# Performance work log

Hardware: AMD Instinct MI355X
Metric: run time of the kernel (lower is better)

## Reference

```python
import jax, jax.numpy as jnp
import numpy as np

N, E, NG = 50000, 800000, 500          # nodes, edges, graphs
HID, HEADS, DH, AIN = 128, 4, 32, 200  # hidden, heads, head dim, atom feat dim
L, NBASE = 5, 1                        # total Roost layers; base layers = roost_layers-3 = 1


def _bn(x, g, b):
    # BatchNorm1d in training mode: batch stats over axis 0 (biased var), affine
    m = x.mean(axis=0)
    v = x.var(axis=0)
    return g * (x - m) * jax.lax.rsqrt(v + 1e-5) + b


def _mlp(x, W, b, g, be):
    # MLPLayer = Linear -> BatchNorm1d -> SiLU
    return jax.nn.silu(_bn(x @ W + b, g, be))


def _roost(x, w, src, dst, Wf, bf, gf, bef, Wg, bg, gg, beg, gn, ben):
    n = x.shape[0]
    hihj = jnp.concatenate([x[src], x[dst]], axis=-1)            # [E, 2h]
    e = jnp.exp(_mlp(hihj, Wf, bf, gf, bef))                     # [E, 1]
    wexp = w[src] * e                                            # [E, 1] src weight * exp(e_ij)
    sum_w = jax.ops.segment_sum(wexp, dst, num_segments=n)       # [N, 1] dst-normalizer
    a = wexp / sum_w[dst]                                        # [E, 1] attention coeff
    z = jnp.einsum('ef,hfd->ehd', hihj, Wg) + bg                 # [E, H, dh] per-head linear
    z = jax.nn.silu(gg * (z - z.mean(axis=0)) * jax.lax.rsqrt(z.var(axis=0) + 1e-5) + beg)
    m = (a[:, :, None] * z).reshape(hihj.shape[0], HID)          # concat heads -> [E, h]
    h = jax.ops.segment_sum(m, dst, num_segments=n)              # scatter-sum to dst nodes
    return _bn(h, gn, ben) + x                                   # bn_nodes + residual


def setup_inputs() -> dict:
    ks = list(jax.random.split(jax.random.key(0), 16))
    f32 = jnp.float32
    return {
        "atom_features": jax.random.normal(ks[0], (N, AIN), f32),
        "node_weight": jax.random.uniform(ks[1], (N, 1), f32, minval=0.05, maxval=1.0),
        "eps": jax.random.normal(ks[2], (N, HID), f32),
        "src": jax.random.randint(ks[3], (E,), 0, N),
        "dst": jax.random.randint(ks[4], (E,), 0, N),
        "graph_ids": jnp.sort(jax.random.randint(ks[5], (N,), 0, NG)),
        "W_embed": jax.random.normal(ks[6], (AIN, HID), f32) / np.sqrt(AIN).astype(np.float32),
        "b_embed": jnp.zeros((HID,), f32),
        "g_embed": jnp.ones((HID,), f32),
        "be_embed": jnp.zeros((HID,), f32),
        "Wf": jax.random.normal(ks[7], (L, 2 * HID, 1), f32) / np.sqrt(2 * HID).astype(np.float32),
        "bf": jnp.zeros((L, 1), f32),
        "gf": jnp.ones((L, 1), f32),
        "bef": jnp.zeros((L, 1), f32),
        "Wg": jax.random.normal(ks[8], (L, HEADS, 2 * HID, DH), f32) / np.sqrt(2 * HID).astype(np.float32),
        "bg": jnp.zeros((L, HEADS, DH), f32),
        "gg": jnp.ones((L, HEADS, DH), f32),
        "beg": jnp.zeros((L, HEADS, DH), f32),
        "gn": jnp.ones((L, HID), f32),
        "ben": jnp.zeros((L, HID), f32),
        "W_mu": jax.random.normal(ks[9], (HID, HID), f32) / np.sqrt(HID).astype(np.float32),
        "b_mu": jnp.zeros((HID,), f32),
        "W_var": jax.random.normal(ks[10], (HID, HID), f32) * 0.01,
        "b_var": jnp.zeros((HID,), f32),
    }


def reference(atom_features, node_weight, eps, W_embed, b_embed, g_embed, be_embed,
              Wf, bf, gf, bef, Wg, bg, gg, beg, gn, ben,
              W_mu, b_mu, W_var, b_var, src, dst, graph_ids):
    x = _mlp(atom_features, W_embed, b_embed, g_embed, be_embed)  # atom_embedding
    for i in range(NBASE):                                        # base_modules
        x = _roost(x, node_weight, src, dst, Wf[i], bf[i], gf[i], bef[i],
                   Wg[i], bg[i], gg[i], beg[i], gn[i], ben[i])
    mu = x @ W_mu + b_mu
    logvar = x @ W_var + b_var
    x = eps * jnp.exp(0.5 * logvar) + mu                          # reparameterize
    for i in range(NBASE, L):                                     # module_layers
        x = _roost(x, node_weight, src, dst, Wf[i], bf[i], gf[i], bef[i],
                   Wg[i], bg[i], gg[i], beg[i], gn[i], ben[i])
    sums = jax.ops.segment_sum(x, graph_ids, num_segments=NG)     # AvgPooling
    cnt = jax.ops.segment_sum(jnp.ones((N,), x.dtype), graph_ids, num_segments=NG)
    xr = sums / jnp.maximum(cnt, 1.0)[:, None]
    kld = jnp.mean(-0.5 * jnp.sum(1.0 + logvar - mu * mu - jnp.exp(logvar), axis=1))
    return xr, kld
```

## Files before the change

kernel.cpp:

```cpp
#include <hip/hip_runtime.h>
#include <hip/hip_bf16.h>
#include <stdint.h>

#define HID 128
#define LAYERS 5

typedef __attribute__((ext_vector_type(8))) short short8;
typedef __attribute__((ext_vector_type(4))) float f32x4;

__device__ __forceinline__ float bf2f(unsigned int u16) {
  union { unsigned int i; float f; } c; c.i = u16 << 16; return c.f;
}
__device__ __forceinline__ unsigned short f2bf(float f) {
  union { float f; unsigned int i; } c; c.f = f;
  unsigned int r = c.i + 0x7fffu + ((c.i >> 16) & 1u);
  return (unsigned short)(r >> 16);
}
__device__ __forceinline__ float fexp(float x) {
  float r; asm("v_exp_f32 %0, %1" : "=v"(r) : "v"(x * 1.44269504f)); return r;
}
__device__ __forceinline__ float frcp(float x) {
  float r; asm("v_rcp_f32 %0, %1" : "=v"(r) : "v"(x)); return r;
}
__device__ __forceinline__ float siluf(float v) { return v * frcp(1.f + fexp(-v)); }

template<int KS, int NCT, bool BF16OUT>
__launch_bounds__(256)
__global__ void gemm_bf16_kernel(const unsigned short* __restrict__ A,
                                 const unsigned short* __restrict__ Bt,
                                 const float* __restrict__ bias,
                                 void* __restrict__ Cv, int M) {
  constexpr int K = KS * 32;
  constexpr int SLOTS = KS * 4;
  constexpr int SSTR = (SLOTS + 7) & ~7;
  __shared__ unsigned short wlds[NCT * 16 * SSTR * 8];
  for (int i = threadIdx.x; i < NCT * 16 * SLOTS; i += 256) {
    int col = i / SLOTS, slot = i % SLOTS;
    int phys = slot ^ (col & 7);
    *(uint4*)&wlds[(col * SSTR + phys) * 8] = *(const uint4*)(Bt + (size_t)col * K + slot * 8);
  }
  __syncthreads();
  int lane = threadIdx.x & 63, wid = threadIdx.x >> 6;
  int l15 = lane & 15, l4 = lane >> 4;
  int n0 = blockIdx.x * 64 + wid * 16;
  f32x4 acc[NCT];
  #pragma unroll
  for (int ct = 0; ct < NCT; ++ct) { f32x4 z = {0.f, 0.f, 0.f, 0.f}; acc[ct] = z; }
  int ar = n0 + l15; if (ar >= M) ar = M - 1;
  #pragma unroll
  for (int kk = 0; kk < KS; ++kk) {
    short8 af = *(const short8*)(A + (size_t)ar * K + kk * 32 + l4 * 8);
    #pragma unroll
    for (int ct = 0; ct < NCT; ++ct) {
      int col = ct * 16 + l15;
      int phys = (kk * 4 + l4) ^ (col & 7);
      short8 bfr = *(const short8*)&wlds[(col * SSTR + phys) * 8];
      acc[ct] = __builtin_amdgcn_mfma_f32_16x16x32_bf16(af, bfr, acc[ct], 0, 0, 0);
    }
  }
  #pragma unroll
  for (int ct = 0; ct < NCT; ++ct) {
    int col = ct * 16 + l15;
    #pragma unroll
    for (int j = 0; j < 4; ++j) {
      int n = n0 + l4 * 4 + j;
      if (n < M) {
        float v = acc[ct][j] + bias[col];
        if (BF16OUT) ((unsigned short*)Cv)[(size_t)n * (NCT * 16) + col] = f2bf(v);
        else         ((float*)Cv)[(size_t)n * (NCT * 16) + col] = v;
      }
    }
  }
}

__global__ void cast_atom_kernel(const float* __restrict__ atom, unsigned short* __restrict__ ab,
                                 int N, int AIN) {
  int n = blockIdx.x, k = threadIdx.x;
  if (n < N && k < 224)
    ab[(size_t)n * 224 + k] = f2bf(k < AIN ? atom[(size_t)n * AIN + k] : 0.f);
}
__global__ void prep_we_kernel(const float* __restrict__ W, unsigned short* __restrict__ Bt,
                               int AIN) {
  int i = blockIdx.x * 256 + threadIdx.x;
  if (i >= 128 * 224) return;
  int col = i / 224, k = i % 224;
  Bt[i] = f2bf(k < AIN ? W[(size_t)k * 128 + col] : 0.f);
}

__global__ void colstats_kernel(const float* __restrict__ in, int M, float* __restrict__ stats) {
  int f = threadIdx.x & 127;
  int rl = threadIdx.x >> 7;
  float s = 0, s2 = 0;
  for (int r = blockIdx.x * 2 + rl; r < M; r += gridDim.x * 2) {
    float v = in[(size_t)r * 128 + f];
    s += v; s2 += v * v;
  }
  __shared__ float l1[256], l2[256];
  l1[threadIdx.x] = s; l2[threadIdx.x] = s2;
  __syncthreads();
  if (rl == 0) {
    atomicAdd(&stats[f],       s  + l1[128 + f]);
    atomicAdd(&stats[128 + f], s2 + l2[128 + f]);
  }
}

template<bool SILU, bool RES>
__global__ void bn_act_kernel(const float* __restrict__ in, const float* __restrict__ stats,
                              const float* __restrict__ g, const float* __restrict__ be,
                              const float* __restrict__ resid, float invM,
                              float* __restrict__ xout, unsigned short* __restrict__ xbout,
                              size_t total) {
  int f = threadIdx.x & 127;
  float mean = stats[f] * invM;
  float var  = stats[128 + f] * invM - mean * mean;
  float sc = g[f] * rsqrtf(var + 1e-5f);
  float sh = be[f] - mean * sc;
  for (size_t i = (size_t)blockIdx.x * blockDim.x + threadIdx.x; i < total;
       i += (size_t)gridDim.x * blockDim.x) {
    float v = in[i] * sc + sh;
    if (SILU) v = siluf(v);
    if (RES)  v += resid[i];
    xout[i] = v;
    xbout[i] = f2bf(v);
  }
}

__global__ void hist_kernel(const int* __restrict__ ids, int* __restrict__ deg, int E) {
  for (int e = blockIdx.x * blockDim.x + threadIdx.x; e < E; e += gridDim.x * blockDim.x)
    atomicAdd(&deg[ids[e]], 1);
}

__global__ void scan_block_kernel(const int* __restrict__ in, int n,
                                  int* __restrict__ excl, int* __restrict__ totals) {
  __shared__ int tmp[256];
  int idx = blockIdx.x * 256 + threadIdx.x;
  int v = (idx < n) ? in[idx] : 0;
  tmp[threadIdx.x] = v;
  __syncthreads();
  for (int o = 1; o < 256; o <<= 1) {
    int t = (threadIdx.x >= o) ? tmp[threadIdx.x - o] : 0;
    __syncthreads();
    tmp[threadIdx.x] += t;
    __syncthreads();
  }
  if (idx < n) excl[idx] = tmp[threadIdx.x] - v;
  if (threadIdx.x == 255 && totals) totals[blockIdx.x] = tmp[255];
}

__global__ void scan_add_kernel(const int* __restrict__ excl, const int* __restrict__ tot_excl,
                                const int* __restrict__ indeg, int* __restrict__ cstart, int n) {
  int idx = blockIdx.x * 256 + threadIdx.x;
  if (idx < n) {
    int v = excl[idx] + tot_excl[blockIdx.x];
    cstart[idx] = v;
    if (idx == n - 1) cstart[n] = v + indeg[idx];
  }
}

__global__ void scatter_kernel(const int* __restrict__ src, const int* __restrict__ dst,
                               const int* __restrict__ cstart, int* __restrict__ fill,
                               int* __restrict__ csrc, int* __restrict__ cdst, int E) {
  for (int e = blockIdx.x * blockDim.x + threadIdx.x; e < E; e += gridDim.x * blockDim.x) {
    int d = dst[e];
    int pos = cstart[d] + atomicAdd(&fill[d], 1);
    csrc[pos] = src[e];
    cdst[pos] = d;
  }
}

__global__ void prep_wg_kernel(const float* __restrict__ WgL, const float* __restrict__ bgL,
                               unsigned short* __restrict__ Bt, float* __restrict__ bias) {
  int i = blockIdx.x * 256 + threadIdx.x;
  if (i < 256 * 128) {
    int col = i >> 7, k = i & 127;
    int c = col & 127, h = c >> 5, d = c & 31;
    int krow = (col < 128) ? k : 128 + k;
    Bt[i] = f2bf(WgL[((size_t)h * 256 + krow) * 32 + d]);
  }
  if (i < 256) bias[i] = (i < 128) ? 0.f : bgL[i - 128];
}

__global__ void prep_mv_kernel(const float* __restrict__ Wm, const float* __restrict__ Wv,
                               const float* __restrict__ bm, const float* __restrict__ bv,
                               unsigned short* __restrict__ Bt, float* __restrict__ bias) {
  int i = blockIdx.x * 256 + threadIdx.x;
  if (i < 256 * 128) {
    int col = i >> 7, k = i & 127;
    Bt[i] = f2bf(col < 128 ? Wm[(size_t)k * 128 + col] : Wv[(size_t)k * 128 + col - 128]);
  }
  if (i < 256) bias[i] = (i < 128) ? bm[i] : bv[i - 128];
}

__global__ void pq_kernel(const float* __restrict__ x, const float* __restrict__ WfL,
                          const float* __restrict__ bfL, float* __restrict__ p,
                          float* __restrict__ q, int N) {
  __shared__ float wf[256];
  wf[threadIdx.x] = WfL[threadIdx.x];
  __syncthreads();
  int wid = threadIdx.x >> 6, lane = threadIdx.x & 63;
  float bf0 = bfL[0];
  for (int n = blockIdx.x * 4 + wid; n < N; n += gridDim.x * 4) {
    float2 xv = *(const float2*)(x + (size_t)n * 128 + lane * 2);
    float pp = xv.x * wf[lane * 2]       + xv.y * wf[lane * 2 + 1];
    float qq = xv.x * wf[128 + lane * 2] + xv.y * wf[129 + lane * 2];
    #pragma unroll
    for (int o = 32; o; o >>= 1) { pp += __shfl_down(pp, o); qq += __shfl_down(qq, o); }
    if (lane == 0) { p[n] = pp; q[n] = qq + bf0; }
  }
}

__global__ void gstat_kernel(const float* __restrict__ p, const float* __restrict__ q,
                             const int* __restrict__ src, const int* __restrict__ dst,
                             float* __restrict__ gstats, int E) {
  float s = 0, s2 = 0;
  for (int e = blockIdx.x * blockDim.x + threadIdx.x; e < E; e += gridDim.x * blockDim.x) {
    float t = p[src[e]] + q[dst[e]];
    s += t; s2 += t * t;
  }
  #pragma unroll
  for (int o = 32; o; o >>= 1) { s += __shfl_down(s, o); s2 += __shfl_down(s2, o); }
  __shared__ float la[4], lb[4];
  int lane = threadIdx.x & 63, wid = threadIdx.x >> 6;
  if (lane == 0) { la[wid] = s; lb[wid] = s2; }
  __syncthreads();
  if (threadIdx.x == 0) {
    atomicAdd(&gstats[0], la[0] + la[1] + la[2] + la[3]);
    atomicAdd(&gstats[1], lb[0] + lb[1] + lb[2] + lb[3]);
  }
}

__global__ void gate_wexp_kernel(const int* __restrict__ cs, const int* __restrict__ csrc,
                                 const float* __restrict__ p, const float* __restrict__ q,
                                 const float* __restrict__ nodew, const float* __restrict__ gstats,
                                 const float* __restrict__ gfL, const float* __restrict__ befL,
                                 float* __restrict__ wexp, float* __restrict__ sum_w,
                                 int N, float invE) {
  float gm  = gstats[0] * invE;
  float gv  = gstats[1] * invE - gm * gm;
  float gsc = gfL[0] * rsqrtf(gv + 1e-5f);
  float gsh = befL[0] - gm * gsc;
  for (int n = blockIdx.x * blockDim.x + threadIdx.x; n < N; n += gridDim.x * blockDim.x) {
    float qn = q[n] * gsc + gsh;
    int s0 = cs[n], s1 = cs[n + 1];
    float sw = 0;
    for (int j = s0; j < s1; ++j) {
      int sn = csrc[j];
      float v = p[sn] * gsc + qn;
      v = v * frcp(1.f + fexp(-v));
      float we = nodew[sn] * fexp(v);
      wexp[j] = we;
      sw += we;
    }
    sum_w[n] = sw;
  }
}

__global__ void zstat_node_kernel(const unsigned short* __restrict__ UVb,
                                  const int* __restrict__ indeg, const int* __restrict__ outdeg,
                                  float* __restrict__ zstats, int N) {
  int lane = threadIdx.x & 63, g = threadIdx.x >> 6;
  int f0 = lane * 2, f1 = f0 + 1;
  float zs0 = 0, zq0 = 0, zs1 = 0, zq1 = 0;
  for (int n = blockIdx.x * 4 + g; n < N; n += gridDim.x * 4) {
    float od = (float)outdeg[n], id = (float)indeg[n];
    unsigned up = *(const unsigned*)(UVb + ((size_t)n << 8) + f0);
    unsigned vp = *(const unsigned*)(UVb + ((size_t)n << 8) + 128 + f0);
    float u0 = bf2f(up & 0xffffu), u1 = bf2f(up >> 16);
    float v0 = bf2f(vp & 0xffffu), v1 = bf2f(vp >> 16);
    zs0 += od * u0 + id * v0;  zq0 += od * u0 * u0 + id * v0 * v0;
    zs1 += od * u1 + id * v1;  zq1 += od * u1 * u1 + id * v1 * v1;
  }
  __shared__ float r1[4][128], r2[4][128];
  r1[g][f0] = zs0; r1[g][f1] = zs1;
  r2[g][f0] = zq0; r2[g][f1] = zq1;
  __syncthreads();
  if (threadIdx.x < 128) {
    int f = threadIdx.x;
    atomicAdd(&zstats[f],       r1[0][f] + r1[1][f] + r1[2][f] + r1[3][f]);
    atomicAdd(&zstats[128 + f], r2[0][f] + r2[1][f] + r2[2][f] + r2[3][f]);
  }
}

__global__ void zcross_kernel(const unsigned short* __restrict__ UVb,
                              const int* __restrict__ csrc, const int* __restrict__ cdst,
                              float* __restrict__ zc_parts, int E) {
  int lane = threadIdx.x & 63;
  int gw = (blockIdx.x * 256 + threadIdx.x) >> 6;
  int nw = (gridDim.x * 256) >> 6;
  int f0 = lane * 2;
  float cr0 = 0, cr1 = 0;
  int nch = (E + 63) >> 6;
  for (int c = gw; c < nch; c += nw) {
    int e0 = c << 6, len = min(64, E - e0);
    int ee = e0 + (lane < len ? lane : len - 1);
    int idxs = csrc[ee], idxd = cdst[ee];
    int dcur = __shfl(idxd, 0);
    float su0 = 0, su1 = 0;
    unsigned up_next = *(const unsigned*)(UVb + ((size_t)__shfl(idxs, 0) << 8) + f0);
    for (int i = 0; i < len; ++i) {
      unsigned up = up_next;
      if (i + 1 < len)
        up_next = *(const unsigned*)(UVb + ((size_t)__shfl(idxs, i + 1) << 8) + f0);
      int d = __shfl(idxd, i);
      if (d != dcur) {
        unsigned vp = *(const unsigned*)(UVb + ((size_t)dcur << 8) + 128 + f0);
        cr0 += bf2f(vp & 0xffffu) * su0; cr1 += bf2f(vp >> 16) * su1;
        su0 = su1 = 0; dcur = d;
      }
      su0 += bf2f(up & 0xffffu); su1 += bf2f(up >> 16);
    }
    unsigned vp = *(const unsigned*)(UVb + ((size_t)dcur << 8) + 128 + f0);
    cr0 += bf2f(vp & 0xffffu) * su0; cr1 += bf2f(vp >> 16) * su1;
  }
  atomicAdd(&zc_parts[(blockIdx.x & 31) * 128 + f0],     cr0);
  atomicAdd(&zc_parts[(blockIdx.x & 31) * 128 + f0 + 1], cr1);
}

__global__ void walk2_kernel(const unsigned short* __restrict__ UVb,
                             const int* __restrict__ csrc, const int* __restrict__ cdst,
                             const float* __restrict__ wexp, const float* __restrict__ sum_w,
                             const float* __restrict__ zstats, const float* __restrict__ zc_parts,
                             const float* __restrict__ gg, const float* __restrict__ beg,
                             float* __restrict__ h, int E, float invE) {
  int lane = threadIdx.x & 63;
  int gw = (blockIdx.x * 256 + threadIdx.x) >> 6;
  int nw = (gridDim.x * 256) >> 6;
  int f0 = lane * 2, f1 = f0 + 1;
  float cr0 = 0, cr1 = 0;
  #pragma unroll
  for (int i2 = 0; i2 < 32; ++i2) { cr0 += zc_parts[i2 * 128 + f0]; cr1 += zc_parts[i2 * 128 + f1]; }
  float zm0 = zstats[f0] * invE;
  float zv0 = (zstats[128 + f0] + 2.f * cr0) * invE - zm0 * zm0;
  float sc0 = gg[f0] * rsqrtf(zv0 + 1e-5f), sh0 = beg[f0] - zm0 * sc0;
  float zm1 = zstats[f1] * invE;
  float zv1 = (zstats[128 + f1] + 2.f * cr1) * invE - zm1 * zm1;
  float sc1 = gg[f1] * rsqrtf(zv1 + 1e-5f), sh1 = beg[f1] - zm1 * sc1;

  int nch = (E + 63) >> 6;
  for (int c = gw; c < nch; c += nw) {
    int e0 = c << 6, len = min(64, E - e0);
    int ee = e0 + (lane < len ? lane : len - 1);
    int idxs = csrc[ee], idxd = cdst[ee];
    float wv = wexp[ee];
    int dcur = __shfl(idxd, 0);
    float inv = frcp(sum_w[dcur]);
    float c0, c1;
    { unsigned vp = *(const unsigned*)(UVb + ((size_t)dcur << 8) + 128 + f0);
      c0 = bf2f(vp & 0xffffu) * sc0 + sh0; c1 = bf2f(vp >> 16) * sc1 + sh1; }
    float h0 = 0, h1 = 0;
    unsigned up_next = *(const unsigned*)(UVb + ((size_t)__shfl(idxs, 0) << 8) + f0);
    for (int i = 0; i < len; ++i) {
      unsigned up = up_next;
      if (i + 1 < len)
        up_next = *(const unsigned*)(UVb + ((size_t)__shfl(idxs, i + 1) << 8) + f0);
      int d = __shfl(idxd, i);
      float a = __shfl(wv, i);
      if (d != dcur) {
        atomicAdd(&h[((size_t)dcur << 7) + f0], h0 * inv);
        atomicAdd(&h[((size_t)dcur << 7) + f1], h1 * inv);
        h0 = h1 = 0; dcur = d; inv = frcp(sum_w[d]);
        unsigned vp = *(const unsigned*)(UVb + ((size_t)d << 8) + 128 + f0);
        c0 = bf2f(vp & 0xffffu) * sc0 + sh0; c1 = bf2f(vp >> 16) * sc1 + sh1;
      }
      float v0 = bf2f(up & 0xffffu) * sc0 + c0;
      float v1 = bf2f(up >> 16)     * sc1 + c1;
      v0 = v0 * frcp(1.f + fexp(-v0));
      v1 = v1 * frcp(1.f + fexp(-v1));
      h0 += a * v0; h1 += a * v1;
    }
    atomicAdd(&h[((size_t)dcur << 7) + f0], h0 * inv);
    atomicAdd(&h[((size_t)dcur << 7) + f1], h1 * inv);
  }
}

__global__ void reparam_kernel(const unsigned short* __restrict__ muv,
                               const float* __restrict__ eps,
                               float* __restrict__ x, unsigned short* __restrict__ xb,
                               float* __restrict__ kacc, size_t total) {
  float part = 0;
  for (size_t i = (size_t)blockIdx.x * blockDim.x + threadIdx.x; i < total;
       i += (size_t)gridDim.x * blockDim.x) {
    size_t n = i >> 7; int f = (int)(i & 127);
    float m = bf2f(muv[(n << 8) + f]);
    float l = bf2f(muv[(n << 8) + 128 + f]);
    float el = fexp(l);
    float v = eps[i] * fexp(0.5f * l) + m;
    x[i] = v;
    xb[i] = f2bf(v);
    part += 1.f + l - m * m - el;
  }
  #pragma unroll
  for (int o = 32; o; o >>= 1) part += __shfl_down(part, o);
  __shared__ float la[4];
  int lane = threadIdx.x & 63, wid = threadIdx.x >> 6;
  if (lane == 0) la[wid] = part;
  __syncthreads();
  if (threadIdx.x == 0) atomicAdd(kacc, la[0] + la[1] + la[2] + la[3]);
}

__global__ void pool_kernel(const float* __restrict__ x, const int* __restrict__ gid,
                            float* __restrict__ pools, float* __restrict__ cnt, size_t total) {
  for (size_t i = (size_t)blockIdx.x * blockDim.x + threadIdx.x; i < total;
       i += (size_t)gridDim.x * blockDim.x) {
    int n = (int)(i >> 7), f = (int)(i & 127);
    int g = gid[n];
    atomicAdd(&pools[(size_t)g * 128 + f], x[i]);
    if (f == 0) atomicAdd(&cnt[g], 1.f);
  }
}

__global__ void finalize_kernel(const float* __restrict__ pools, const float* __restrict__ cnt,
                                const float* __restrict__ kacc, float* __restrict__ out,
                                int NG, float invN) {
  int i = blockIdx.x * blockDim.x + threadIdx.x;
  if (i < NG * 128) {
    float c = cnt[i >> 7];
    c = c > 1.f ? c : 1.f;
    out[i] = pools[i] / c;
  }
  if (i == 0) out[NG * 128] = -0.5f * kacc[0] * invN;
}

extern "C" void kernel_launch(void* const* d_in, const int* in_sizes, int n_in,
                              void* d_out, int out_size, void* d_ws, size_t ws_size,
                              hipStream_t stream) {
  const float* atom    = (const float*)d_in[0];
  const float* nodew   = (const float*)d_in[1];
  const float* epsp    = (const float*)d_in[2];
  const int*   src     = (const int*)d_in[3];
  const int*   dst     = (const int*)d_in[4];
  const int*   gid     = (const int*)d_in[5];
  const float* W_embed = (const float*)d_in[6];
  const float* b_embed = (const float*)d_in[7];
  const float* g_embed = (const float*)d_in[8];
  const float* be_embed= (const float*)d_in[9];
  const float* Wf      = (const float*)d_in[10];
  const float* bfp     = (const float*)d_in[11];
  const float* gfp     = (const float*)d_in[12];
  const float* befp    = (const float*)d_in[13];
  const float* Wg      = (const float*)d_in[14];
  const float* bg      = (const float*)d_in[15];
  const float* gg      = (const float*)d_in[16];
  const float* beg     = (const float*)d_in[17];
  const float* gn      = (const float*)d_in[18];
  const float* ben     = (const float*)d_in[19];
  const float* W_mu    = (const float*)d_in[20];
  const float* b_mu    = (const float*)d_in[21];
  const float* W_var   = (const float*)d_in[22];
  const float* b_var   = (const float*)d_in[23];

  const int N   = in_sizes[1];
  const int E   = in_sizes[3];
  const int AIN = in_sizes[0] / N;
  const int NG  = (out_size - 1) / HID;

  char* w = (char*)d_ws;
  size_t off = 0;
  auto alloc = [&](size_t bytes) { size_t r = off; off = (off + bytes + 255) & ~(size_t)255; return r; };
  size_t o_x    = alloc((size_t)N*HID*4);
  size_t o_xb   = alloc((size_t)N*HID*2);
  size_t o_uvb  = alloc((size_t)N*256*2);
  size_t o_h    = alloc((size_t)N*HID*4);
  size_t o_ab   = alloc((size_t)N*224*2);
  size_t o_p    = alloc((size_t)N*4);
  size_t o_q    = alloc((size_t)N*4);
  size_t o_sw   = alloc((size_t)N*4);
  size_t o_wexp = alloc((size_t)E*4);
  size_t o_csrc = alloc((size_t)E*4);
  size_t o_cdst = alloc((size_t)E*4);
  size_t o_cs   = alloc((size_t)(N+1)*4);
  size_t o_deg  = alloc((size_t)3*N*4);
  size_t o_excl = alloc((size_t)N*4);
  size_t o_tot  = alloc(512*4);
  size_t o_bt   = alloc((size_t)256*128*2);
  size_t o_bias = alloc(256*4);
  size_t o_st   = alloc((514 + 32*128)*4);
  size_t o_kp   = alloc((size_t)(64 + NG*HID + NG)*4);

  float* x              = (float*)(w + o_x);
  unsigned short* xb    = (unsigned short*)(w + o_xb);
  unsigned short* UVb   = (unsigned short*)(w + o_uvb);
  float* h              = (float*)(w + o_h);
  unsigned short* atomb = (unsigned short*)(w + o_ab);
  float* p              = (float*)(w + o_p);
  float* q              = (float*)(w + o_q);
  float* sum_w          = (float*)(w + o_sw);
  float* wexp           = (float*)(w + o_wexp);
  int*   csrc           = (int*)(w + o_csrc);
  int*   cdst           = (int*)(w + o_cdst);
  int*   cstart         = (int*)(w + o_cs);
  int*   indeg          = (int*)(w + o_deg);
  int*   fill           = indeg + N;
  int*   outdeg         = indeg + 2*N;
  int*   excl           = (int*)(w + o_excl);
  int*   totals         = (int*)(w + o_tot);
  int*   tot_excl       = totals + 256;
  unsigned short* Bt    = (unsigned short*)(w + o_bt);
  float* bias           = (float*)(w + o_bias);
  float* stats          = (float*)(w + o_st);
  float* gstats         = stats;
  float* zstats         = stats + 2;
  float* nstats         = stats + 258;
  float* zc_parts       = stats + 514;
  float* kacc           = (float*)(w + o_kp);
  float* pools          = kacc + 64;
  float* cnt            = pools + (size_t)NG*HID;

  const dim3 B(256);
  const int mblk = (N + 63) / 64;
  const int nb1  = (N + 255) / 256;
  const float invN = 1.f / (float)N;
  const float invE = 1.f / (float)E;
  const size_t totalNH = (size_t)N * HID;
  const size_t st_bytes = (514 + 32*128) * 4;

  hipMemsetAsync(w + o_st, 0, st_bytes, stream);
  hipMemsetAsync(w + o_kp, 0, (64 + (size_t)NG*HID + NG)*4, stream);
  hipMemsetAsync(w + o_deg, 0, (size_t)3*N*4, stream);

  hist_kernel<<<dim3(1024), B, 0, stream>>>(dst, indeg, E);
  hist_kernel<<<dim3(1024), B, 0, stream>>>(src, outdeg, E);
  scan_block_kernel<<<dim3(nb1), B, 0, stream>>>(indeg, N, excl, totals);
  scan_block_kernel<<<dim3(1), B, 0, stream>>>(totals, nb1, tot_excl, nullptr);
  scan_add_kernel<<<dim3(nb1), B, 0, stream>>>(excl, tot_excl, indeg, cstart, N);
  scatter_kernel<<<dim3(1024), B, 0, stream>>>(src, dst, cstart, fill, csrc, cdst, E);

  cast_atom_kernel<<<dim3(N), B, 0, stream>>>(atom, atomb, N, AIN);
  prep_we_kernel<<<dim3(112), B, 0, stream>>>(W_embed, Bt, AIN);
  gemm_bf16_kernel<7, 8, false><<<dim3(mblk), B, 0, stream>>>(atomb, Bt, b_embed, h, N);
  colstats_kernel<<<dim3(512), B, 0, stream>>>(h, N, nstats);
  bn_act_kernel<true,false><<<dim3(2048), B, 0, stream>>>(h, nstats, g_embed, be_embed,
                                                          x, invN, x, xb, totalNH);

  for (int l = 0; l < LAYERS; ++l) {
    if (l == 1) {
      prep_mv_kernel<<<dim3(128), B, 0, stream>>>(W_mu, W_var, b_mu, b_var, Bt, bias);
      gemm_bf16_kernel<4, 16, true><<<dim3(mblk), B, 0, stream>>>(xb, Bt, bias, UVb, N);
      reparam_kernel<<<dim3(2048), B, 0, stream>>>(UVb, epsp, x, xb, kacc, totalNH);
    }
    prep_wg_kernel<<<dim3(128), B, 0, stream>>>(Wg + (size_t)l*4*256*32, bg + l*128, Bt, bias);
    hipMemsetAsync(w + o_st, 0, st_bytes, stream);
    hipMemsetAsync(w + o_h, 0, (size_t)N*HID*4, stream);
    gemm_bf16_kernel<4, 16, true><<<dim3(mblk), B, 0, stream>>>(xb, Bt, bias, UVb, N);
    pq_kernel<<<dim3(2048), B, 0, stream>>>(x, Wf + l*256, bfp + l, p, q, N);
    gstat_kernel<<<dim3(1024), B, 0, stream>>>(p, q, src, dst, gstats, E);
    gate_wexp_kernel<<<dim3(256), B, 0, stream>>>(cstart, csrc, p, q, nodew, gstats,
                                                  gfp + l, befp + l, wexp, sum_w, N, invE);
    zstat_node_kernel<<<dim3(512), B, 0, stream>>>(UVb, indeg, outdeg, zstats, N);
    zcross_kernel<<<dim3(2048), B, 0, stream>>>(UVb, csrc, cdst, zc_parts, E);
    walk2_kernel<<<dim3(2048), B, 0, stream>>>(UVb, csrc, cdst, wexp, sum_w, zstats, zc_parts,
                                               gg + l*128, beg + l*128, h, E, invE);
    colstats_kernel<<<dim3(512), B, 0, stream>>>(h, N, nstats);
    bn_act_kernel<false,true><<<dim3(2048), B, 0, stream>>>(h, nstats, gn + l*128, ben + l*128,
                                                            x, invN, x, xb, totalNH);
  }

  pool_kernel<<<dim3(1024), B, 0, stream>>>(x, gid, pools, cnt, totalNH);
  finalize_kernel<<<dim3((NG*HID + 255)/256), B, 0, stream>>>(pools, cnt, kacc,
                                                              (float*)d_out, NG, invN);
}
```

Measured before the change: 2.168 ms.

## Fold gate statistics into node and edge walks, unroll gathers, segment-reduce pooling

The separate per-edge gate-statistics pass is removed. The mean and variance of p[src]+q[dst] are now computed algebraically: degree-weighted node sums are taken in pq_kernel, and the cross term p*q is accumulated inside the existing edge walk, renamed xwalk. The gate/wexp kernel becomes edge-parallel with atomic accumulation into sum_w, and the edge walks are unrolled by four to keep more gathers in flight. Pooling now exploits the sorted graph ids and reduces contiguous runs before issuing atomics. In exchange, pq reads the bf16 copy of x, which loses precision in the gate logits, and the added atomics on sum_w can contend.

Measured after the change: 3.368 ms. +55.4%, slower.

```diff
diff --git a/kernel.cpp b/kernel.cpp
--- a/kernel.cpp
+++ b/kernel.cpp
@@ -191,67 +191,35 @@
   if (i < 256) bias[i] = (i < 128) ? bm[i] : bv[i - 128];
 }
 
-__global__ void pq_kernel(const float* __restrict__ x, const float* __restrict__ WfL,
-                          const float* __restrict__ bfL, float* __restrict__ p,
-                          float* __restrict__ q, int N) {
+__global__ void pq_kernel(const unsigned short* __restrict__ xb, const float* __restrict__ WfL,
+                          const float* __restrict__ bfL, const int* __restrict__ indeg,
+                          const int* __restrict__ outdeg, float* __restrict__ p,
+                          float* __restrict__ q, float* __restrict__ gstats, int N) {
   __shared__ float wf[256];
   wf[threadIdx.x] = WfL[threadIdx.x];
   __syncthreads();
   int wid = threadIdx.x >> 6, lane = threadIdx.x & 63;
+  int f0 = lane * 2;
   float bf0 = bfL[0];
+  float t1 = 0, t2 = 0;
   for (int n = blockIdx.x * 4 + wid; n < N; n += gridDim.x * 4) {
-    float2 xv = *(const float2*)(x + (size_t)n * 128 + lane * 2);
-    float pp = xv.x * wf[lane * 2]       + xv.y * wf[lane * 2 + 1];
-    float qq = xv.x * wf[128 + lane * 2] + xv.y * wf[129 + lane * 2];
+    unsigned xv = *(const unsigned*)(xb + ((size_t)n << 7) + f0);
+    float x0 = bf2f(xv & 0xffffu), x1 = bf2f(xv >> 16);
+    float pp = x0 * wf[f0]       + x1 * wf[f0 + 1];
+    float qq = x0 * wf[128 + f0] + x1 * wf[129 + f0];
     #pragma unroll
     for (int o = 32; o; o >>= 1) { pp += __shfl_down(pp, o); qq += __shfl_down(qq, o); }
-    if (lane == 0) { p[n] = pp; q[n] = qq + bf0; }
-  }
-}
-
-__global__ void gstat_kernel(const float* __restrict__ p, const float* __restrict__ q,
-                             const int* __restrict__ src, const int* __restrict__ dst,
-                             float* __restrict__ gstats, int E) {
-  float s = 0, s2 = 0;
-  for (int e = blockIdx.x * blockDim.x + threadIdx.x; e < E; e += gridDim.x * blockDim.x) {
-    float t = p[src[e]] + q[dst[e]];
-    s += t; s2 += t * t;
-  }
-  #pragma unroll
-  for (int o = 32; o; o >>= 1) { s += __shfl_down(s, o); s2 += __shfl_down(s2, o); }
-  __shared__ float la[4], lb[4];
-  int lane = threadIdx.x & 63, wid = threadIdx.x >> 6;
-  if (lane == 0) { la[wid] = s; lb[wid] = s2; }
-  __syncthreads();
-  if (threadIdx.x == 0) {
-    atomicAdd(&gstats[0], la[0] + la[1] + la[2] + la[3]);
-    atomicAdd(&gstats[1], lb[0] + lb[1] + lb[2] + lb[3]);
-  }
-}
-
-__global__ void gate_wexp_kernel(const int* __restrict__ cs, const int* __restrict__ csrc,
-                                 const float* __restrict__ p, const float* __restrict__ q,
-                                 const float* __restrict__ nodew, const float* __restrict__ gstats,
-                                 const float* __restrict__ gfL, const float* __restrict__ befL,
-                                 float* __restrict__ wexp, float* __restrict__ sum_w,
-                                 int N, float invE) {
-  float gm  = gstats[0] * invE;
-  float gv  = gstats[1] * invE - gm * gm;
-  float gsc = gfL[0] * rsqrtf(gv + 1e-5f);
-  float gsh = befL[0] - gm * gsc;
-  for (int n = blockIdx.x * blockDim.x + threadIdx.x; n < N; n += gridDim.x * blockDim.x) {
-    float qn = q[n] * gsc + gsh;
-    int s0 = cs[n], s1 = cs[n + 1];
-    float sw = 0;
-    for (int j = s0; j < s1; ++j) {
-      int sn = csrc[j];
-      float v = p[sn] * gsc + qn;
-      v = v * frcp(1.f + fexp(-v));
-      float we = nodew[sn] * fexp(v);
-      wexp[j] = we;
-      sw += we;
-    }
-    sum_w[n] = sw;
+    if (lane == 0) {
+      qq += bf0;
+      p[n] = pp; q[n] = qq;
+      float od = (float)outdeg[n], id = (float)indeg[n];
+      t1 += od * pp + id * qq;
+      t2 += od * pp * pp + id * qq * qq;
+    }
+  }
+  if (lane == 0) {
+    atomicAdd(&gstats[0], t1);
+    atomicAdd(&gstats[1], t2);
   }
 }
 
@@ -281,39 +249,69 @@
   }
 }
 
-__global__ void zcross_kernel(const unsigned short* __restrict__ UVb,
-                              const int* __restrict__ csrc, const int* __restrict__ cdst,
-                              float* __restrict__ zc_parts, int E) {
+__global__ void xwalk_kernel(const unsigned short* __restrict__ UVb,
+                             const int* __restrict__ csrc, const int* __restrict__ cdst,
+                             const float* __restrict__ p, const float* __restrict__ q,
+                             float* __restrict__ zc_parts, float* __restrict__ gstats, int E) {
   int lane = threadIdx.x & 63;
   int gw = (blockIdx.x * 256 + threadIdx.x) >> 6;
   int nw = (gridDim.x * 256) >> 6;
   int f0 = lane * 2;
-  float cr0 = 0, cr1 = 0;
+  float cr0 = 0, cr1 = 0, gc = 0;
   int nch = (E + 63) >> 6;
   for (int c = gw; c < nch; c += nw) {
     int e0 = c << 6, len = min(64, E - e0);
     int ee = e0 + (lane < len ? lane : len - 1);
     int idxs = csrc[ee], idxd = cdst[ee];
+    if (lane < len) gc += p[idxs] * q[idxd];
     int dcur = __shfl(idxd, 0);
     float su0 = 0, su1 = 0;
-    unsigned up_next = *(const unsigned*)(UVb + ((size_t)__shfl(idxs, 0) << 8) + f0);
-    for (int i = 0; i < len; ++i) {
-      unsigned up = up_next;
-      if (i + 1 < len)
-        up_next = *(const unsigned*)(UVb + ((size_t)__shfl(idxs, i + 1) << 8) + f0);
-      int d = __shfl(idxd, i);
-      if (d != dcur) {
-        unsigned vp = *(const unsigned*)(UVb + ((size_t)dcur << 8) + 128 + f0);
-        cr0 += bf2f(vp & 0xffffu) * su0; cr1 += bf2f(vp >> 16) * su1;
-        su0 = su1 = 0; dcur = d;
-      }
-      su0 += bf2f(up & 0xffffu); su1 += bf2f(up >> 16);
-    }
-    unsigned vp = *(const unsigned*)(UVb + ((size_t)dcur << 8) + 128 + f0);
+    const unsigned short* base = UVb;
+    #define LDU(i) (*(const unsigned*)(base + ((size_t)__shfl(idxs, (i) < len ? (i) : len - 1) << 8) + f0))
+    unsigned a0 = LDU(0), a1 = LDU(1), a2 = LDU(2), a3 = LDU(3);
+    for (int bs = 0; bs < len; bs += 4) {
+      unsigned b0 = LDU(bs + 4), b1 = LDU(bs + 5), b2 = LDU(bs + 6), b3 = LDU(bs + 7);
+      #define PROCX(i, up) if ((i) < len) {                                        \
+        int d = __shfl(idxd, (i));                                                 \
+        if (d != dcur) {                                                           \
+          unsigned vp = *(const unsigned*)(base + ((size_t)dcur << 8) + 128 + f0); \
+          cr0 += bf2f(vp & 0xffffu) * su0; cr1 += bf2f(vp >> 16) * su1;            \
+          su0 = su1 = 0; dcur = d;                                                 \
+        }                                                                          \
+        su0 += bf2f((up) & 0xffffu); su1 += bf2f((up) >> 16); }
+      PROCX(bs + 0, a0); PROCX(bs + 1, a1); PROCX(bs + 2, a2); PROCX(bs + 3, a3);
+      a0 = b0; a1 = b1; a2 = b2; a3 = b3;
+    }
+    unsigned vp = *(const unsigned*)(base + ((size_t)dcur << 8) + 128 + f0);
     cr0 += bf2f(vp & 0xffffu) * su0; cr1 += bf2f(vp >> 16) * su1;
+    #undef PROCX
+    #undef LDU
   }
   atomicAdd(&zc_parts[(blockIdx.x & 31) * 128 + f0],     cr0);
   atomicAdd(&zc_parts[(blockIdx.x & 31) * 128 + f0 + 1], cr1);
+  #pragma unroll
+  for (int o = 32; o; o >>= 1) gc += __shfl_down(gc, o);
+  if (lane == 0) atomicAdd(&gstats[2], gc);
+}
+
+__global__ void gate_wexp_kernel(const int* __restrict__ csrc, const int* __restrict__ cdst,
+                                 const float* __restrict__ p, const float* __restrict__ q,
+                                 const float* __restrict__ nodew, const float* __restrict__ gstats,
+                                 const float* __restrict__ gfL, const float* __restrict__ befL,
+                                 float* __restrict__ wexp, float* __restrict__ sum_w,
+                                 int E, float invE) {
+  float gm  = gstats[0] * invE;
+  float gv  = (gstats[1] + 2.f * gstats[2]) * invE - gm * gm;
+  float gsc = gfL[0] * rsqrtf(gv + 1e-5f);
+  float gsh = befL[0] - gm * gsc;
+  for (int e = blockIdx.x * blockDim.x + threadIdx.x; e < E; e += gridDim.x * blockDim.x) {
+    int s = csrc[e], d = cdst[e];
+    float v = (p[s] + q[d]) * gsc + gsh;
+    v = v * frcp(1.f + fexp(-v));
+    float we = nodew[s] * fexp(v);
+    wexp[e] = we;
+    atomicAdd(&sum_w[d], we);
+  }
 }
 
 __global__ void walk2_kernel(const unsigned short* __restrict__ UVb,
@@ -348,28 +346,32 @@
     { unsigned vp = *(const unsigned*)(UVb + ((size_t)dcur << 8) + 128 + f0);
       c0 = bf2f(vp & 0xffffu) * sc0 + sh0; c1 = bf2f(vp >> 16) * sc1 + sh1; }
     float h0 = 0, h1 = 0;
-    unsigned up_next = *(const unsigned*)(UVb + ((size_t)__shfl(idxs, 0) << 8) + f0);
-    for (int i = 0; i < len; ++i) {
-      unsigned up = up_next;
-      if (i + 1 < len)
-        up_next = *(const unsigned*)(UVb + ((size_t)__shfl(idxs, i + 1) << 8) + f0);
-      int d = __shfl(idxd, i);
-      float a = __shfl(wv, i);
-      if (d != dcur) {
-        atomicAdd(&h[((size_t)dcur << 7) + f0], h0 * inv);
-        atomicAdd(&h[((size_t)dcur << 7) + f1], h1 * inv);
-        h0 = h1 = 0; dcur = d; inv = frcp(sum_w[d]);
-        unsigned vp = *(const unsigned*)(UVb + ((size_t)d << 8) + 128 + f0);
-        c0 = bf2f(vp & 0xffffu) * sc0 + sh0; c1 = bf2f(vp >> 16) * sc1 + sh1;
-      }
-      float v0 = bf2f(up & 0xffffu) * sc0 + c0;
-      float v1 = bf2f(up >> 16)     * sc1 + c1;
-      v0 = v0 * frcp(1.f + fexp(-v0));
-      v1 = v1 * frcp(1.f + fexp(-v1));
-      h0 += a * v0; h1 += a * v1;
+    #define LDU(i) (*(const unsigned*)(UVb + ((size_t)__shfl(idxs, (i) < len ? (i) : len - 1) << 8) + f0))
+    unsigned a0 = LDU(0), a1 = LDU(1), a2 = LDU(2), a3 = LDU(3);
+    for (int bs = 0; bs < len; bs += 4) {
+      unsigned b0 = LDU(bs + 4), b1 = LDU(bs + 5), b2 = LDU(bs + 6), b3 = LDU(bs + 7);
+      #define PROCW(i, up) if ((i) < len) {                                          \
+        int d = __shfl(idxd, (i));                                                   \
+        float a = __shfl(wv, (i));                                                   \
+        if (d != dcur) {                                                             \
+          atomicAdd(&h[((size_t)dcur << 7) + f0], h0 * inv);                         \
+          atomicAdd(&h[((size_t)dcur << 7) + f1], h1 * inv);                         \
+          h0 = h1 = 0; dcur = d; inv = frcp(sum_w[d]);                               \
+          unsigned vp = *(const unsigned*)(UVb + ((size_t)d << 8) + 128 + f0);       \
+          c0 = bf2f(vp & 0xffffu) * sc0 + sh0; c1 = bf2f(vp >> 16) * sc1 + sh1;      \
+        }                                                                            \
+        float v0 = bf2f((up) & 0xffffu) * sc0 + c0;                                  \
+        float v1 = bf2f((up) >> 16)     * sc1 + c1;                                  \
+        v0 = v0 * frcp(1.f + fexp(-v0));                                             \
+        v1 = v1 * frcp(1.f + fexp(-v1));                                             \
+        h0 += a * v0; h1 += a * v1; }
+      PROCW(bs + 0, a0); PROCW(bs + 1, a1); PROCW(bs + 2, a2); PROCW(bs + 3, a3);
+      a0 = b0; a1 = b1; a2 = b2; a3 = b3;
     }
     atomicAdd(&h[((size_t)dcur << 7) + f0], h0 * inv);
     atomicAdd(&h[((size_t)dcur << 7) + f1], h1 * inv);
+    #undef PROCW
+    #undef LDU
   }
 }
 
@@ -399,13 +401,31 @@
 }
 
 __global__ void pool_kernel(const float* __restrict__ x, const int* __restrict__ gid,
-                            float* __restrict__ pools, float* __restrict__ cnt, size_t total) {
-  for (size_t i = (size_t)blockIdx.x * blockDim.x + threadIdx.x; i < total;
-       i += (size_t)gridDim.x * blockDim.x) {
-    int n = (int)(i >> 7), f = (int)(i & 127);
-    int g = gid[n];
-    atomicAdd(&pools[(size_t)g * 128 + f], x[i]);
-    if (f == 0) atomicAdd(&cnt[g], 1.f);
+                            float* __restrict__ pools, float* __restrict__ cnt, int N) {
+  int lane = threadIdx.x & 63;
+  int gw = (blockIdx.x * 256 + threadIdx.x) >> 6;
+  int nw = (gridDim.x * 256) >> 6;
+  int f0 = lane * 2, f1 = f0 + 1;
+  const int CH = 64;
+  int nch = (N + CH - 1) / CH;
+  for (int c = gw; c < nch; c += nw) {
+    int n0 = c * CH, n1 = min(N, n0 + CH);
+    int gcur = gid[n0];
+    float a0 = 0, a1 = 0, count = 0;
+    for (int n = n0; n < n1; ++n) {
+      int g = gid[n];
+      if (g != gcur) {
+        atomicAdd(&pools[((size_t)gcur << 7) + f0], a0);
+        atomicAdd(&pools[((size_t)gcur << 7) + f1], a1);
+        if (lane == 0) atomicAdd(&cnt[gcur], count);
+        a0 = a1 = 0; count = 0; gcur = g;
+      }
+      float2 xv = *(const float2*)(x + ((size_t)n << 7) + f0);
+      a0 += xv.x; a1 += xv.y; count += 1.f;
+    }
+    atomicAdd(&pools[((size_t)gcur << 7) + f0], a0);
+    atomicAdd(&pools[((size_t)gcur << 7) + f1], a1);
+    if (lane == 0) atomicAdd(&cnt[gcur], count);
   }
 }
 
@@ -474,7 +494,7 @@
   size_t o_tot  = alloc(512*4);
   size_t o_bt   = alloc((size_t)256*128*2);
   size_t o_bias = alloc(256*4);
-  size_t o_st   = alloc((514 + 32*128)*4);
+  size_t o_st   = alloc((516 + 32*128)*4);
   size_t o_kp   = alloc((size_t)(64 + NG*HID + NG)*4);
 
   float* x              = (float*)(w + o_x);
@@ -499,9 +519,9 @@
   float* bias           = (float*)(w + o_bias);
   float* stats          = (float*)(w + o_st);
   float* gstats         = stats;
-  float* zstats         = stats + 2;
-  float* nstats         = stats + 258;
-  float* zc_parts       = stats + 514;
+  float* zstats         = stats + 4;
+  float* nstats         = stats + 260;
+  float* zc_parts       = stats + 516;
   float* kacc           = (float*)(w + o_kp);
   float* pools          = kacc + 64;
   float* cnt            = pools + (size_t)NG*HID;
@@ -512,7 +532,7 @@
   const float invN = 1.f / (float)N;
   const float invE = 1.f / (float)E;
   const size_t totalNH = (size_t)N * HID;
-  const size_t st_bytes = (514 + 32*128) * 4;
+  const size_t st_bytes = (516 + 32*128) * 4;
 
   hipMemsetAsync(w + o_st, 0, st_bytes, stream);
   hipMemsetAsync(w + o_kp, 0, (64 + (size_t)NG*HID + NG)*4, stream);
@@ -541,13 +561,14 @@
     prep_wg_kernel<<<dim3(128), B, 0, stream>>>(Wg + (size_t)l*4*256*32, bg + l*128, Bt, bias);
     hipMemsetAsync(w + o_st, 0, st_bytes, stream);
     hipMemsetAsync(w + o_h, 0, (size_t)N*HID*4, stream);
+    hipMemsetAsync(w + o_sw, 0, (size_t)N*4, stream);
     gemm_bf16_kernel<4, 16, true><<<dim3(mblk), B, 0, stream>>>(xb, Bt, bias, UVb, N);
-    pq_kernel<<<dim3(2048), B, 0, stream>>>(x, Wf + l*256, bfp + l, p, q, N);
-    gstat_kernel<<<dim3(1024), B, 0, stream>>>(p, q, src, dst, gstats, E);
-    gate_wexp_kernel<<<dim3(256), B, 0, stream>>>(cstart, csrc, p, q, nodew, gstats,
-                                                  gfp + l, befp + l, wexp, sum_w, N, invE);
+    pq_kernel<<<dim3(2048), B, 0, stream>>>(xb, Wf + l*256, bfp + l, indeg, outdeg,
+                                            p, q, gstats, N);
+    xwalk_kernel<<<dim3(2048), B, 0, stream>>>(UVb, csrc, cdst, p, q, zc_parts, gstats, E);
     zstat_node_kernel<<<dim3(512), B, 0, stream>>>(UVb, indeg, outdeg, zstats, N);
-    zcross_kernel<<<dim3(2048), B, 0, stream>>>(UVb, csrc, cdst, zc_parts, E);
+    gate_wexp_kernel<<<dim3(1024), B, 0, stream>>>(csrc, cdst, p, q, nodew, gstats,
+                                                   gfp + l, befp + l, wexp, sum_w, E, invE);
     walk2_kernel<<<dim3(2048), B, 0, stream>>>(UVb, csrc, cdst, wexp, sum_w, zstats, zc_parts,
                                                gg + l*128, beg + l*128, h, E, invE);
     colstats_kernel<<<dim3(512), B, 0, stream>>>(h, N, nstats);
@@ -555,7 +576,7 @@
                                                             x, invN, x, xb, totalNH);
   }
 
-  pool_kernel<<<dim3(1024), B, 0, stream>>>(x, gid, pools, cnt, totalNH);
+  pool_kernel<<<dim3(256), B, 0, stream>>>(x, gid, pools, cnt, N);
   finalize_kernel<<<dim3((NG*HID + 255)/256), B, 0, stream>>>(pools, cnt, kacc,
                                                               (float*)d_out, NG, invN);
 }
```
